# Kernel tuning notes

Hardware: AMD Instinct MI355X
Metric: run time of the kernel (lower is better)

The kernel has to match this reference:

```python
import jax, jax.numpy as jnp
import numpy as np

HIDDEN = 1024
HEADS = 16
HEAD_DIM = HIDDEN // HEADS  # 64
B, S = 2, 2048


def setup_inputs() -> dict:
    key = jax.random.key(0)
    ks = jax.random.split(key, 12)
    lim_h = 1.0 / np.sqrt(HEAD_DIM)
    lim_o = 1.0 / np.sqrt(HIDDEN)
    u = lambda k, shape, lim: jax.random.uniform(k, shape, jnp.float32, -lim, lim)
    return {
        "query": jax.random.normal(ks[0], (B, S, HIDDEN), jnp.float32),
        "key": jax.random.normal(ks[1], (B, S, HIDDEN), jnp.float32),
        "value": jax.random.normal(ks[2], (B, S, HIDDEN), jnp.float32),
        "mask": jax.random.randint(ks[3], (B, 1, S, S), 0, 2, jnp.int32),
        "Wq": u(ks[4], (HEAD_DIM, HEAD_DIM), lim_h), "bq": u(ks[5], (HEAD_DIM,), lim_h),
        "Wk": u(ks[6], (HEAD_DIM, HEAD_DIM), lim_h), "bk": u(ks[7], (HEAD_DIM,), lim_h),
        "Wv": u(ks[8], (HEAD_DIM, HEAD_DIM), lim_h), "bv": u(ks[9], (HEAD_DIM,), lim_h),
        "Wo": u(ks[10], (HIDDEN, HIDDEN), lim_o), "bo": u(ks[11], (HIDDEN,), lim_o),
    }


def reference(query, key, value, mask, Wq, bq, Wk, bk, Wv, bv, Wo, bo):
    b = query.shape[0]
    # view [B, S, H, D]; per-head linear is SHARED across heads (head_dim x head_dim)
    q = query.reshape(b, -1, HEADS, HEAD_DIM) @ Wq.T + bq
    k = key.reshape(b, -1, HEADS, HEAD_DIM) @ Wk.T + bk
    v = value.reshape(b, -1, HEADS, HEAD_DIM) @ Wv.T + bv
    scores = jnp.einsum('nqhd,nkhd->nhqk', q, k)  # [B, H, Sq, Sk]
    scores = jnp.where(mask == 0, jnp.float32(-1e20), scores)
    # NOTE: original scales by sqrt(hidden_dim), not sqrt(head_dim)
    attn = jax.nn.softmax(scores / np.sqrt(HIDDEN).astype(np.float32), axis=3)
    out = jnp.einsum('nhql,nlhd->nqhd', attn, v).reshape(b, query.shape[1], HIDDEN)
    return out @ Wo.T + bo
```

## Files before the change

### kernel.cpp

```cpp
#include <hip/hip_runtime.h>
#include <hip/hip_bf16.h>

#define NB 2
#define NS 2048
#define NH 16
#define ND 64
#define NHID 1024

#define QSCALE 0.045084220f

typedef __attribute__((ext_vector_type(8))) short bf16x8;
typedef __attribute__((ext_vector_type(4))) short s16x4;
typedef __attribute__((ext_vector_type(4))) float f32x4;

typedef __attribute__((address_space(3))) unsigned int lds_u32;
typedef __attribute__((address_space(1))) unsigned int glb_u32;

__device__ inline void gl_lds16(const void* g, void* l) {
  __builtin_amdgcn_global_load_lds((const glb_u32*)g, (lds_u32*)l, 16, 0, 0);
}

__device__ inline short f2bf(float f) {
  __hip_bfloat16 h = __float2bfloat16(f);
  short s; __builtin_memcpy(&s, &h, 2); return s;
}

__device__ inline float selbit(float e, unsigned long long m) {
  float r;
  asm("v_cndmask_b32 %0, 0, %1, %2" : "=v"(r) : "v"(e), "s"(m));
  return r;
}

__device__ inline bf16x8 cvt8(const float* __restrict__ p) {
  float4 x = *(const float4*)p;
  float4 y = *(const float4*)(p + 4);
  bf16x8 r;
  r[0] = f2bf(x.x); r[1] = f2bf(x.y); r[2] = f2bf(x.z); r[3] = f2bf(x.w);
  r[4] = f2bf(y.x); r[5] = f2bf(y.y); r[6] = f2bf(y.z); r[7] = f2bf(y.w);
  return r;
}

__global__ __launch_bounds__(256) void prep(
    const int* __restrict__ mask, unsigned long long* __restrict__ mp,
    const float* __restrict__ Wq, const float* __restrict__ Wk,
    const float* __restrict__ Wv, const float* __restrict__ Wo,
    short* __restrict__ Wq_b, short* __restrict__ Wk_b,
    short* __restrict__ Wv_b, short* __restrict__ Wo_b)
{
  if (blockIdx.x < 512) {
    int tg = blockIdx.x * 256 + threadIdx.x;
    int q4 = tg & 3;
    int g4 = tg >> 2;
    int mt = g4 & 3, kt = (g4 >> 2) & 31, qg = (g4 >> 7) & 127, b = g4 >> 14;
    unsigned long long wq[4] = {0ull, 0ull, 0ull, 0ull};
#pragma unroll
    for (int cc = 0; cc < 4; ++cc) {
      int c2 = q4 * 4 + cc;
      const int4* p = (const int4*)(mask +
          ((size_t)(b * NS + qg * 16 + c2) * NS) + kt * 64 + mt * 16);
#pragma unroll
      for (int qq2 = 0; qq2 < 4; ++qq2) {
        int4 v = p[qq2];
        int sh = qq2 * 16 + c2;
        wq[0] |= (unsigned long long)(v.x != 0) << sh;
        wq[1] |= (unsigned long long)(v.y != 0) << sh;
        wq[2] |= (unsigned long long)(v.z != 0) << sh;
        wq[3] |= (unsigned long long)(v.w != 0) << sh;
      }
    }
#pragma unroll
    for (int r = 0; r < 4; ++r) {
      wq[r] |= __shfl_xor(wq[r], 1);
      wq[r] |= __shfl_xor(wq[r], 2);
    }
    mp[(size_t)g4 * 4 + q4] = wq[q4];
  } else {
    int i = ((blockIdx.x - 512) * 256 + threadIdx.x) * 4;
    const float* src; short* dst; int off; float sc = 1.0f;
    if (i < 1048576)      { src = Wo; dst = Wo_b; off = i; }
    else {
      int j = i - 1048576;
      if (j < 4096)       { src = Wq; dst = Wq_b; off = j; sc = QSCALE; }
      else if (j < 8192)  { src = Wk; dst = Wk_b; off = j - 4096; }
      else                { src = Wv; dst = Wv_b; off = j - 8192; }
    }
    float4 v = *(const float4*)(src + off);
    s16x4 o;
    o[0] = f2bf(v.x * sc); o[1] = f2bf(v.y * sc);
    o[2] = f2bf(v.z * sc); o[3] = f2bf(v.w * sc);
    *(s16x4*)(dst + off) = o;
  }
}

__global__ __launch_bounds__(256) void qk_proj(
    const float* __restrict__ qin, const float* __restrict__ kin,
    const short* __restrict__ Wq_b, const float* __restrict__ bq,
    const short* __restrict__ Wk_b, const float* __restrict__ bk,
    short* __restrict__ Qws, short* __restrict__ Kws)
{
  __shared__ __align__(16) short ldsT[4][16][72];
  const int tid = threadIdx.x;
  const int w = tid >> 6, lane = tid & 63;
  const int c = lane & 15, qq = lane >> 4;
  const int t = blockIdx.x * 4 + w;
  const int b = t >> 11, s = t & (NS - 1);
  const int aoff = (t * 16 + c) * 64 + qq * 8;
  const int row0 = lane >> 3, inner = lane & 7;

#pragma unroll
  for (int m = 0; m < 2; ++m) {
    const float* X  = (m == 0) ? qin  : kin;
    const short* W  = (m == 0) ? Wq_b : Wk_b;
    const float* bb = (m == 0) ? bq   : bk;
    short* dst      = (m == 0) ? Qws  : Kws;
    const float bsc = (m == 0) ? QSCALE : 1.0f;

    bf16x8 a0 = cvt8(X + aoff);
    bf16x8 a1 = cvt8(X + aoff + 32);

#pragma unroll
    for (int nt = 0; nt < 4; ++nt) {
      f32x4 z = {0.f, 0.f, 0.f, 0.f};
      const short* wp = W + (nt * 16 + c) * 64 + qq * 8;
      bf16x8 b0 = *(const bf16x8*)(wp);
      bf16x8 b1 = *(const bf16x8*)(wp + 32);
      z = __builtin_amdgcn_mfma_f32_16x16x32_bf16(a0, b0, z, 0, 0, 0);
      z = __builtin_amdgcn_mfma_f32_16x16x32_bf16(a1, b1, z, 0, 0, 0);
      float bias = bb[nt * 16 + c] * bsc;
#pragma unroll
      for (int r = 0; r < 4; ++r)
        ldsT[w][qq * 4 + r][nt * 16 + c] = f2bf(z[r] + bias);
    }

    bf16x8 v0 = *(const bf16x8*)&ldsT[w][row0][inner * 8];
    bf16x8 v1 = *(const bf16x8*)&ldsT[w][row0 + 8][inner * 8];
    int bh0 = b * NH + row0, bh1 = b * NH + row0 + 8;
    *(bf16x8*)(dst + (bh0 * NS + s) * 64 + inner * 8) = v0;
    *(bf16x8*)(dst + (bh1 * NS + s) * 64 + inner * 8) = v1;
  }
}

__global__ __launch_bounds__(256) void vproj(
    const float* __restrict__ vin, const short* __restrict__ Wv_b,
    const float* __restrict__ bv, short* __restrict__ Vt)
{
  __shared__ __align__(16) short ldsVT[64][72];
  const int tid = threadIdx.x;
  const int g = tid >> 6, lane = tid & 63;
  const int c = lane & 15, qq = lane >> 4;
  const int bh = blockIdx.x >> 5;
  const int stile = blockIdx.x & 31;
  const int b = bh >> 4, h = bh & 15;
  const int sb = stile * 64;

  bf16x8 wv[8];
  float bias[4];
#pragma unroll
  for (int nt = 0; nt < 4; ++nt) {
    const short* wp = Wv_b + (nt * 16 + c) * 64 + qq * 8;
    wv[nt * 2]     = *(const bf16x8*)(wp);
    wv[nt * 2 + 1] = *(const bf16x8*)(wp + 32);
    bias[nt] = bv[nt * 16 + c];
  }

  const float* ap = vin + ((size_t)((b * NS + sb + 16 * g + c) * 16 + h)) * 64 + qq * 8;
  bf16x8 a0 = cvt8(ap);
  bf16x8 a1 = cvt8(ap + 32);
#pragma unroll
  for (int nt = 0; nt < 4; ++nt) {
    f32x4 z = {0.f, 0.f, 0.f, 0.f};
    z = __builtin_amdgcn_mfma_f32_16x16x32_bf16(a0, wv[nt * 2], z, 0, 0, 0);
    z = __builtin_amdgcn_mfma_f32_16x16x32_bf16(a1, wv[nt * 2 + 1], z, 0, 0, 0);
    ushort4 u;
    u.x = (unsigned short)f2bf(z[0] + bias[nt]);
    u.y = (unsigned short)f2bf(z[1] + bias[nt]);
    u.z = (unsigned short)f2bf(z[2] + bias[nt]);
    u.w = (unsigned short)f2bf(z[3] + bias[nt]);
    *(ushort4*)&ldsVT[nt * 16 + c][16 * g + qq * 4] = u;
  }
  __syncthreads();

#pragma unroll
  for (int j = 0; j < 2; ++j) {
    int idx = tid + 256 * j;
    int d = idx >> 3, unit = idx & 7;
    bf16x8 o = *(const bf16x8*)&ldsVT[d][unit * 8];
    *(bf16x8*)(Vt + ((size_t)(bh * 64 + d)) * NS + sb + unit * 8) = o;
  }
}

__global__ __launch_bounds__(256, 4) void attn(
    const short* __restrict__ Qws, const short* __restrict__ Kws,
    const short* __restrict__ Vt, const unsigned long long* __restrict__ Mp,
    short* __restrict__ AO)
{
  __shared__ __align__(16) short Ks[2][64][64];
  __shared__ __align__(16) short Vs[2][64][64];
  __shared__ __align__(16) short Ps[4][16][64];

  const int tid = threadIdx.x;
  const int w = tid >> 6, lane = tid & 63;
  const int c = lane & 15, qq = lane >> 4;
  const int bh = blockIdx.x & 31;
  const int qtile = blockIdx.x >> 5;
  const int b = bh >> 4, h = bh & 15;
  const int qbase = qtile * 64 + w * 16;
  const int ca2 = (lane & 7) << 1;

  const short* Qp = Qws + (size_t)bh * (NS * 64);
  const short* Kp = Kws + (size_t)bh * (NS * 64);
  const short* Vp = Vt + (size_t)bh * (64 * NS);

  const int wu = __builtin_amdgcn_readfirstlane(w);
  const unsigned long long* mbase =
      Mp + (size_t)(b * (NS / 16) + qtile * 4 + wu) * ((NS / 64) * 16);

  bf16x8 aq0, aq1;
  {
    const short* qp = Qp + (qbase + c) * 64 + qq * 8;
    aq0 = *(const bf16x8*)(qp);
    aq1 = *(const bf16x8*)(qp + 32);
  }

  float lsum = 0.f;
  f32x4 O[4];
#pragma unroll
  for (int dt = 0; dt < 4; ++dt) { f32x4 z = {0.f, 0.f, 0.f, 0.f}; O[dt] = z; }

  short* Pw = &Ps[w][c][0];

  const int srow = lane >> 3;
  const int sunit = (lane & 7) ^ srow;
  auto stage = [&](int kt, int buf) {
#pragma unroll
    for (int i = 0; i < 2; ++i) {
      int j = w * 2 + i;
      const short* gk = Kp + ((size_t)(kt * 64 + j * 8 + srow)) * 64 + sunit * 8;
      gl_lds16(gk, &Ks[buf][0][0] + j * 512);
      const short* gv = Vp + ((size_t)(j * 8 + srow)) * NS + kt * 64 + sunit * 8;
      gl_lds16(gv, &Vs[buf][0][0] + j * 512);
    }
  };

  stage(0, 0);
  __syncthreads();

  for (int kt = 0; kt < NS / 64; ++kt) {
    const int buf = kt & 1;
    if (kt < NS / 64 - 1) stage(kt + 1, buf ^ 1);

    unsigned long long mw[16];
#pragma unroll
    for (int i = 0; i < 16; ++i) mw[i] = mbase[(size_t)kt * 16 + i];

    f32x4 st[4];
#pragma unroll
    for (int mt = 0; mt < 4; ++mt) {
      const short* kb = &Ks[buf][mt * 16 + c][0];
      bf16x8 ak0 = *(const bf16x8*)(kb + ((qq ^ (c & 7)) << 3));
      bf16x8 ak1 = *(const bf16x8*)(kb + (((4 + qq) ^ (c & 7)) << 3));
      f32x4 z = {0.f, 0.f, 0.f, 0.f};
      z = __builtin_amdgcn_mfma_f32_16x16x32_bf16(ak0, aq0, z, 0, 0, 0);
      z = __builtin_amdgcn_mfma_f32_16x16x32_bf16(ak1, aq1, z, 0, 0, 0);
      st[mt] = z;
    }

#pragma unroll
    for (int mt = 0; mt < 4; ++mt) {
      f32x4 s = st[mt];
      float e0 = selbit(__builtin_amdgcn_exp2f(s[0]), mw[mt * 4 + 0]);
      float e1 = selbit(__builtin_amdgcn_exp2f(s[1]), mw[mt * 4 + 1]);
      float e2 = selbit(__builtin_amdgcn_exp2f(s[2]), mw[mt * 4 + 2]);
      float e3 = selbit(__builtin_amdgcn_exp2f(s[3]), mw[mt * 4 + 3]);
      lsum += (e0 + e1) + (e2 + e3);
      ushort4 u;
      u.x = (unsigned short)f2bf(e0);
      u.y = (unsigned short)f2bf(e1);
      u.z = (unsigned short)f2bf(e2);
      u.w = (unsigned short)f2bf(e3);
      *(ushort4*)&Pw[((mt * 4 + qq) ^ ca2) << 2] = u;
    }

#pragma unroll
    for (int ks = 0; ks < 2; ++ks) {
      bf16x8 pf = *(const bf16x8*)&Pw[((ks * 8 + qq * 2) ^ ca2) << 2];
#pragma unroll
      for (int dt = 0; dt < 4; ++dt) {
        const short* vb = &Vs[buf][dt * 16 + c][0];
        bf16x8 vf = *(const bf16x8*)(vb + ((((ks << 2) + qq) ^ (c & 7)) << 3));
        O[dt] = __builtin_amdgcn_mfma_f32_16x16x32_bf16(vf, pf, O[dt], 0, 0, 0);
      }
    }

    __syncthreads();
  }

  {
    float v = lsum;
    v += __shfl_xor(v, 16);
    v += __shfl_xor(v, 32);
    lsum = 1.0f / fmaxf(v, 1e-30f);
  }

  const int row = qbase + c;
#pragma unroll
  for (int dt = 0; dt < 4; ++dt) {
    ushort4 u;
    u.x = (unsigned short)f2bf(O[dt][0] * lsum);
    u.y = (unsigned short)f2bf(O[dt][1] * lsum);
    u.z = (unsigned short)f2bf(O[dt][2] * lsum);
    u.w = (unsigned short)f2bf(O[dt][3] * lsum);
    *(ushort4*)(AO + ((size_t)(b * NS + row)) * NHID + h * 64 + dt * 16 + qq * 4) = u;
  }
}

__global__ __launch_bounds__(256, 2) void oproj(
    const short* __restrict__ X, const short* __restrict__ Wo_b,
    const float* __restrict__ bo, float* __restrict__ out)
{
  __shared__ __align__(16) short As[2][64][64];
  __shared__ __align__(16) short Bs[2][128][64];
  const int tid = threadIdx.x;
  const int w = tid >> 6, lane = tid & 63;
  const int c = lane & 15, qq = lane >> 4;
  const int rowbase = blockIdx.x * 64;
  const int colbase = blockIdx.y * 128;
  const int mh = w & 1, nh = w >> 1;

  const int srow = lane >> 3;
  const int sunit = (lane & 7) ^ srow;

  auto stage = [&](int kb, int buf) {
#pragma unroll
    for (int i = 0; i < 6; ++i) {
      int t = w * 6 + i;
      if (t < 8) {
        const short* g = X + (size_t)(rowbase + t * 8 + srow) * NHID
                           + kb * 64 + sunit * 8;
        gl_lds16(g, &As[buf][0][0] + t * 512);
      } else {
        int j = t - 8;
        const short* g = Wo_b + (size_t)(colbase + j * 8 + srow) * NHID
                              + kb * 64 + sunit * 8;
        gl_lds16(g, &Bs[buf][0][0] + j * 512);
      }
    }
  };

  f32x4 acc[2][4];
#pragma unroll
  for (int mt = 0; mt < 2; ++mt)
#pragma unroll
    for (int nt = 0; nt < 4; ++nt) { f32x4 z = {0.f, 0.f, 0.f, 0.f}; acc[mt][nt] = z; }

  stage(0, 0);
  __syncthreads();

  for (int kb = 0; kb < NHID / 64; ++kb) {
    const int buf = kb & 1;
    if (kb < NHID / 64 - 1) stage(kb + 1, buf ^ 1);

    bf16x8 af[2][2];
#pragma unroll
    for (int mt = 0; mt < 2; ++mt) {
      const short* ap = &As[buf][mh * 32 + mt * 16 + c][0];
#pragma unroll
      for (int ks = 0; ks < 2; ++ks)
        af[mt][ks] = *(const bf16x8*)(ap + ((((ks << 2) + qq) ^ (c & 7)) << 3));
    }
#pragma unroll
    for (int nt = 0; nt < 4; ++nt) {
      const short* bp = &Bs[buf][nh * 64 + nt * 16 + c][0];
#pragma unroll
      for (int ks = 0; ks < 2; ++ks) {
        bf16x8 bf = *(const bf16x8*)(bp + ((((ks << 2) + qq) ^ (c & 7)) << 3));
#pragma unroll
        for (int mt = 0; mt < 2; ++mt)
          acc[mt][nt] = __builtin_amdgcn_mfma_f32_16x16x32_bf16(af[mt][ks], bf, acc[mt][nt], 0, 0, 0);
      }
    }

    __syncthreads();
  }

#pragma unroll
  for (int nt = 0; nt < 4; ++nt) {
    int col = colbase + nh * 64 + nt * 16 + c;
    float bias = bo[col];
#pragma unroll
    for (int mt = 0; mt < 2; ++mt) {
      int row = rowbase + mh * 32 + mt * 16 + qq * 4;
#pragma unroll
      for (int r = 0; r < 4; ++r)
        out[(size_t)(row + r) * NHID + col] = acc[mt][nt][r] + bias;
    }
  }
}

extern "C" void kernel_launch(void* const* d_in, const int* in_sizes, int n_in,
                              void* d_out, int out_size, void* d_ws, size_t ws_size,
                              hipStream_t stream) {
  const float* qin = (const float*)d_in[0];
  const float* kin = (const float*)d_in[1];
  const float* vin = (const float*)d_in[2];
  const int*  mask = (const int*)d_in[3];
  const float* Wq = (const float*)d_in[4];
  const float* bq = (const float*)d_in[5];
  const float* Wk = (const float*)d_in[6];
  const float* bk = (const float*)d_in[7];
  const float* Wv = (const float*)d_in[8];
  const float* bv = (const float*)d_in[9];
  const float* Wo = (const float*)d_in[10];
  const float* bo = (const float*)d_in[11];
  float* out = (float*)d_out;

  char* ws = (char*)d_ws;
  short* Qws = (short*)(ws);
  short* Kws = (short*)(ws + (size_t)(8 << 20));
  short* Vt  = (short*)(ws + (size_t)(16 << 20));
  short* AO  = (short*)(ws + (size_t)(24 << 20));
  unsigned long long* Mp = (unsigned long long*)(ws + (size_t)(32 << 20));
  short* Wo_b = (short*)(ws + (size_t)(33 << 20));
  short* Wq_b = (short*)(ws + (size_t)(35 << 20));
  short* Wk_b = (short*)(ws + (size_t)(35 << 20) + 8192);
  short* Wv_b = (short*)(ws + (size_t)(35 << 20) + 16384);

  prep<<<1548, 256, 0, stream>>>(mask, Mp, Wq, Wk, Wv, Wo, Wq_b, Wk_b, Wv_b, Wo_b);
  qk_proj<<<NB * NS / 4, 256, 0, stream>>>(qin, kin, Wq_b, bq, Wk_b, bk, Qws, Kws);
  vproj<<<(NB * NH) * (NS / 64), 256, 0, stream>>>(vin, Wv_b, bv, Vt);
  attn<<<(NB * NH) * (NS / 64), 256, 0, stream>>>(Qws, Kws, Vt, Mp, AO);
  oproj<<<dim3(64, 8), 256, 0, stream>>>(AO, Wo_b, bo, out);
}
```

Before: 212.5 us.

## Merge QK and V projections into one launch, add MFMA priority hints, retune prep/oproj

Combines the qk_proj and vproj kernels into a single qkv_proj launch that branches on block index, removing one kernel launch and the gap between the two. The attention loop wraps its MFMA sections in s_setprio to favour matrix issue across waves. The mask bit-packing in prep is remapped so the four lanes that cooperate are 16 apart, making the mask reads across a wavefront more contiguous. The oproj occupancy hint is raised from 2 to 3 blocks per CU, which may increase register pressure or spilling.

After: 210.4 us. About the same (-1.0%).

```diff
diff --git a/kernel.cpp b/kernel.cpp
--- a/kernel.cpp
+++ b/kernel.cpp
@@ -48,9 +48,10 @@
     short* __restrict__ Wv_b, short* __restrict__ Wo_b)
 {
   if (blockIdx.x < 512) {
-    int tg = blockIdx.x * 256 + threadIdx.x;
-    int q4 = tg & 3;
-    int g4 = tg >> 2;
+    int idx = blockIdx.x * 256 + threadIdx.x;
+    int lane = threadIdx.x & 63;
+    int q4 = lane >> 4;
+    int g4 = ((idx >> 6) << 4) | (lane & 15);
     int mt = g4 & 3, kt = (g4 >> 2) & 31, qg = (g4 >> 7) & 127, b = g4 >> 14;
     unsigned long long wq[4] = {0ull, 0ull, 0ull, 0ull};
 #pragma unroll
@@ -70,8 +71,8 @@
     }
 #pragma unroll
     for (int r = 0; r < 4; ++r) {
-      wq[r] |= __shfl_xor(wq[r], 1);
-      wq[r] |= __shfl_xor(wq[r], 2);
+      wq[r] |= __shfl_xor(wq[r], 16);
+      wq[r] |= __shfl_xor(wq[r], 32);
     }
     mp[(size_t)g4 * 4 + q4] = wq[q4];
   } else {
@@ -92,100 +93,100 @@
   }
 }
 
-__global__ __launch_bounds__(256) void qk_proj(
+__global__ __launch_bounds__(256) void qkv_proj(
     const float* __restrict__ qin, const float* __restrict__ kin,
+    const float* __restrict__ vin,
     const short* __restrict__ Wq_b, const float* __restrict__ bq,
     const short* __restrict__ Wk_b, const float* __restrict__ bk,
-    short* __restrict__ Qws, short* __restrict__ Kws)
+    const short* __restrict__ Wv_b, const float* __restrict__ bv,
+    short* __restrict__ Qws, short* __restrict__ Kws, short* __restrict__ Vt)
 {
-  __shared__ __align__(16) short ldsT[4][16][72];
+  __shared__ __align__(16) short lds[4][16][72];
   const int tid = threadIdx.x;
-  const int w = tid >> 6, lane = tid & 63;
-  const int c = lane & 15, qq = lane >> 4;
-  const int t = blockIdx.x * 4 + w;
-  const int b = t >> 11, s = t & (NS - 1);
-  const int aoff = (t * 16 + c) * 64 + qq * 8;
-  const int row0 = lane >> 3, inner = lane & 7;
-
-#pragma unroll
-  for (int m = 0; m < 2; ++m) {
-    const float* X  = (m == 0) ? qin  : kin;
-    const short* W  = (m == 0) ? Wq_b : Wk_b;
-    const float* bb = (m == 0) ? bq   : bk;
-    short* dst      = (m == 0) ? Qws  : Kws;
-    const float bsc = (m == 0) ? QSCALE : 1.0f;
-
-    bf16x8 a0 = cvt8(X + aoff);
-    bf16x8 a1 = cvt8(X + aoff + 32);
-
+
+  if (blockIdx.x < NB * NS / 4) {
+    const int w = tid >> 6, lane = tid & 63;
+    const int c = lane & 15, qq = lane >> 4;
+    const int t = blockIdx.x * 4 + w;
+    const int b = t >> 11, s = t & (NS - 1);
+    const int aoff = (t * 16 + c) * 64 + qq * 8;
+    const int row0 = lane >> 3, inner = lane & 7;
+
+#pragma unroll
+    for (int m = 0; m < 2; ++m) {
+      const float* X  = (m == 0) ? qin  : kin;
+      const short* W  = (m == 0) ? Wq_b : Wk_b;
+      const float* bb = (m == 0) ? bq   : bk;
+      short* dst      = (m == 0) ? Qws  : Kws;
+      const float bsc = (m == 0) ? QSCALE : 1.0f;
+
+      bf16x8 a0 = cvt8(X + aoff);
+      bf16x8 a1 = cvt8(X + aoff + 32);
+
+#pragma unroll
+      for (int nt = 0; nt < 4; ++nt) {
+        f32x4 z = {0.f, 0.f, 0.f, 0.f};
+        const short* wp = W + (nt * 16 + c) * 64 + qq * 8;
+        bf16x8 b0 = *(const bf16x8*)(wp);
+        bf16x8 b1 = *(const bf16x8*)(wp + 32);
+        z = __builtin_amdgcn_mfma_f32_16x16x32_bf16(a0, b0, z, 0, 0, 0);
+        z = __builtin_amdgcn_mfma_f32_16x16x32_bf16(a1, b1, z, 0, 0, 0);
+        float bias = bb[nt * 16 + c] * bsc;
+#pragma unroll
+        for (int r = 0; r < 4; ++r)
+          lds[w][qq * 4 + r][nt * 16 + c] = f2bf(z[r] + bias);
+      }
+
+      bf16x8 v0 = *(const bf16x8*)&lds[w][row0][inner * 8];
+      bf16x8 v1 = *(const bf16x8*)&lds[w][row0 + 8][inner * 8];
+      int bh0 = b * NH + row0, bh1 = b * NH + row0 + 8;
+      *(bf16x8*)(dst + (bh0 * NS + s) * 64 + inner * 8) = v0;
+      *(bf16x8*)(dst + (bh1 * NS + s) * 64 + inner * 8) = v1;
+    }
+  } else {
+    short (*ldsVT)[72] = (short (*)[72])lds;
+    const int bid = blockIdx.x - NB * NS / 4;
+    const int g = tid >> 6, lane = tid & 63;
+    const int c = lane & 15, qq = lane >> 4;
+    const int bh = bid >> 5;
+    const int stile = bid & 31;
+    const int b = bh >> 4, h = bh & 15;
+    const int sb = stile * 64;
+
+    bf16x8 wv[8];
+    float bias[4];
+#pragma unroll
+    for (int nt = 0; nt < 4; ++nt) {
+      const short* wp = Wv_b + (nt * 16 + c) * 64 + qq * 8;
+      wv[nt * 2]     = *(const bf16x8*)(wp);
+      wv[nt * 2 + 1] = *(const bf16x8*)(wp + 32);
+      bias[nt] = bv[nt * 16 + c];
+    }
+
+    const float* ap = vin + ((size_t)((b * NS + sb + 16 * g + c) * 16 + h)) * 64 + qq * 8;
+    bf16x8 a0 = cvt8(ap);
+    bf16x8 a1 = cvt8(ap + 32);
 #pragma unroll
     for (int nt = 0; nt < 4; ++nt) {
       f32x4 z = {0.f, 0.f, 0.f, 0.f};
-      const short* wp = W + (nt * 16 + c) * 64 + qq * 8;
-      bf16x8 b0 = *(const bf16x8*)(wp);
-      bf16x8 b1 = *(const bf16x8*)(wp + 32);
-      z = __builtin_amdgcn_mfma_f32_16x16x32_bf16(a0, b0, z, 0, 0, 0);
-      z = __builtin_amdgcn_mfma_f32_16x16x32_bf16(a1, b1, z, 0, 0, 0);
-      float bias = bb[nt * 16 + c] * bsc;
-#pragma unroll
-      for (int r = 0; r < 4; ++r)
-        ldsT[w][qq * 4 + r][nt * 16 + c] = f2bf(z[r] + bias);
-    }
-
-    bf16x8 v0 = *(const bf16x8*)&ldsT[w][row0][inner * 8];
-    bf16x8 v1 = *(const bf16x8*)&ldsT[w][row0 + 8][inner * 8];
-    int bh0 = b * NH + row0, bh1 = b * NH + row0 + 8;
-    *(bf16x8*)(dst + (bh0 * NS + s) * 64 + inner * 8) = v0;
-    *(bf16x8*)(dst + (bh1 * NS + s) * 64 + inner * 8) = v1;
-  }
-}
-
-__global__ __launch_bounds__(256) void vproj(
-    const float* __restrict__ vin, const short* __restrict__ Wv_b,
-    const float* __restrict__ bv, short* __restrict__ Vt)
-{
-  __shared__ __align__(16) short ldsVT[64][72];
-  const int tid = threadIdx.x;
-  const int g = tid >> 6, lane = tid & 63;
-  const int c = lane & 15, qq = lane >> 4;
-  const int bh = blockIdx.x >> 5;
-  const int stile = blockIdx.x & 31;
-  const int b = bh >> 4, h = bh & 15;
-  const int sb = stile * 64;
-
-  bf16x8 wv[8];
-  float bias[4];
-#pragma unroll
-  for (int nt = 0; nt < 4; ++nt) {
-    const short* wp = Wv_b + (nt * 16 + c) * 64 + qq * 8;
-    wv[nt * 2]     = *(const bf16x8*)(wp);
-    wv[nt * 2 + 1] = *(const bf16x8*)(wp + 32);
-    bias[nt] = bv[nt * 16 + c];
-  }
-
-  const float* ap = vin + ((size_t)((b * NS + sb + 16 * g + c) * 16 + h)) * 64 + qq * 8;
-  bf16x8 a0 = cvt8(ap);
-  bf16x8 a1 = cvt8(ap + 32);
-#pragma unroll
-  for (int nt = 0; nt < 4; ++nt) {
-    f32x4 z = {0.f, 0.f, 0.f, 0.f};
-    z = __builtin_amdgcn_mfma_f32_16x16x32_bf16(a0, wv[nt * 2], z, 0, 0, 0);
-    z = __builtin_amdgcn_mfma_f32_16x16x32_bf16(a1, wv[nt * 2 + 1], z, 0, 0, 0);
-    ushort4 u;
-    u.x = (unsigned short)f2bf(z[0] + bias[nt]);
-    u.y = (unsigned short)f2bf(z[1] + bias[nt]);
-    u.z = (unsigned short)f2bf(z[2] + bias[nt]);
-    u.w = (unsigned short)f2bf(z[3] + bias[nt]);
-    *(ushort4*)&ldsVT[nt * 16 + c][16 * g + qq * 4] = u;
-  }
-  __syncthreads();
-
-#pragma unroll
-  for (int j = 0; j < 2; ++j) {
-    int idx = tid + 256 * j;
-    int d = idx >> 3, unit = idx & 7;
-    bf16x8 o = *(const bf16x8*)&ldsVT[d][unit * 8];
-    *(bf16x8*)(Vt + ((size_t)(bh * 64 + d)) * NS + sb + unit * 8) = o;
+      z = __builtin_amdgcn_mfma_f32_16x16x32_bf16(a0, wv[nt * 2], z, 0, 0, 0);
+      z = __builtin_amdgcn_mfma_f32_16x16x32_bf16(a1, wv[nt * 2 + 1], z, 0, 0, 0);
+      ushort4 u;
+      u.x = (unsigned short)f2bf(z[0] + bias[nt]);
+      u.y = (unsigned short)f2bf(z[1] + bias[nt]);
+      u.z = (unsigned short)f2bf(z[2] + bias[nt]);
+      u.w = (unsigned short)f2bf(z[3] + bias[nt]);
+      *(ushort4*)&ldsVT[nt * 16 + c][16 * g + qq * 4] = u;
+    }
+    __syncthreads();
+
+#pragma unroll
+    for (int j = 0; j < 2; ++j) {
+      int idx = tid + 256 * j;
+      int d = idx >> 3, unit = idx & 7;
+      bf16x8 o = *(const bf16x8*)&ldsVT[d][unit * 8];
+      *(bf16x8*)(Vt + ((size_t)(bh * 64 + d)) * NS + sb + unit * 8) = o;
+    }
   }
 }
 
@@ -254,6 +255,7 @@
     for (int i = 0; i < 16; ++i) mw[i] = mbase[(size_t)kt * 16 + i];
 
     f32x4 st[4];
+    __builtin_amdgcn_s_setprio(1);
 #pragma unroll
     for (int mt = 0; mt < 4; ++mt) {
       const short* kb = &Ks[buf][mt * 16 + c][0];
@@ -264,6 +266,7 @@
       z = __builtin_amdgcn_mfma_f32_16x16x32_bf16(ak1, aq1, z, 0, 0, 0);
       st[mt] = z;
     }
+    __builtin_amdgcn_s_setprio(0);
 
 #pragma unroll
     for (int mt = 0; mt < 4; ++mt) {
@@ -281,6 +284,7 @@
       *(ushort4*)&Pw[((mt * 4 + qq) ^ ca2) << 2] = u;
     }
 
+    __builtin_amdgcn_s_setprio(1);
 #pragma unroll
     for (int ks = 0; ks < 2; ++ks) {
       bf16x8 pf = *(const bf16x8*)&Pw[((ks * 8 + qq * 2) ^ ca2) << 2];
@@ -291,6 +295,7 @@
         O[dt] = __builtin_amdgcn_mfma_f32_16x16x32_bf16(vf, pf, O[dt], 0, 0, 0);
       }
     }
+    __builtin_amdgcn_s_setprio(0);
 
     __syncthreads();
   }
@@ -314,7 +319,7 @@
   }
 }
 
-__global__ __launch_bounds__(256, 2) void oproj(
+__global__ __launch_bounds__(256, 3) void oproj(
     const short* __restrict__ X, const short* __restrict__ Wo_b,
     const float* __restrict__ bo, float* __restrict__ out)
 {
@@ -426,8 +431,8 @@
   short* Wv_b = (short*)(ws + (size_t)(35 << 20) + 16384);
 
   prep<<<1548, 256, 0, stream>>>(mask, Mp, Wq, Wk, Wv, Wo, Wq_b, Wk_b, Wv_b, Wo_b);
-  qk_proj<<<NB * NS / 4, 256, 0, stream>>>(qin, kin, Wq_b, bq, Wk_b, bk, Qws, Kws);
-  vproj<<<(NB * NH) * (NS / 64), 256, 0, stream>>>(vin, Wv_b, bv, Vt);
+  qkv_proj<<<NB * NS / 4 + (NB * NH) * (NS / 64), 256, 0, stream>>>(
+      qin, kin, vin, Wq_b, bq, Wk_b, bk, Wv_b, bv, Qws, Kws, Vt);
   attn<<<(NB * NH) * (NS / 64), 256, 0, stream>>>(Qws, Kws, Vt, Mp, AO);
   oproj<<<dim3(64, 8), 256, 0, stream>>>(AO, Wo_b, bo, out);
 }
```
